# Kernel optimization log

Measured on AMD Instinct MI355X. Metric: run time of the kernel, lower is better.

Reference implementation:

```python
import jax, jax.numpy as jnp
import numpy as np

N_NODES = 50000
N_EDGES = 800000
VOCAB = 4096          # node_emb_size
EMB_DIM = 128         # node_emb_dim
HIDDEN = 128          # hidden_dim -> layer1 out = 2*HIDDEN
N_POS = 1024


def gcn_conv(h, edge_index, W, b, n):
    """PyG GCNConv: lin -> add self loops -> sym-normalized scatter-add -> +bias."""
    h = h @ W                                   # [N, out]
    row, col = edge_index[0], edge_index[1]     # source, target
    loop = jnp.arange(n)
    row = jnp.concatenate([row, loop])
    col = jnp.concatenate([col, loop])
    deg = jax.ops.segment_sum(jnp.ones(row.shape[0], dtype=h.dtype), col, num_segments=n)
    dinv = jnp.where(deg > 0, jax.lax.rsqrt(deg), 0.0)
    norm = dinv[row] * dinv[col]                # [E+N]
    msg = h[row] * norm[:, None]                # gather + scale
    return jax.ops.segment_sum(msg, col, num_segments=n) + b


def setup_inputs() -> dict:
    key = jax.random.key(0)
    ks = jax.random.split(key, 10)
    x = jax.random.randint(ks[0], (N_NODES, 1), 0, VOCAB)
    edge_index = jax.random.randint(ks[1], (2, N_EDGES), 0, N_NODES)
    x_position = jax.random.randint(ks[2], (N_POS,), 0, N_NODES)
    # Embedding init: normal(0, emb_dim^-0.5) per initialize_parameters
    emb = jax.random.normal(ks[3], (VOCAB, EMB_DIM), jnp.float32) * EMB_DIM ** -0.5
    # GCN / linear weights (glorot-ish)
    W1 = jax.random.normal(ks[4], (EMB_DIM, 2 * HIDDEN), jnp.float32) * (EMB_DIM ** -0.5)
    b1 = jnp.zeros((2 * HIDDEN,), jnp.float32)
    W2 = jax.random.normal(ks[5], (2 * HIDDEN, HIDDEN), jnp.float32) * ((2 * HIDDEN) ** -0.5)
    b2 = jnp.zeros((HIDDEN,), jnp.float32)
    Wc = jax.random.normal(ks[6], (HIDDEN, VOCAB), jnp.float32) * (HIDDEN ** -0.5)
    bc = jnp.zeros((VOCAB,), jnp.float32)
    return {"x": x, "edge_index": edge_index, "x_position": x_position,
            "emb": emb, "W1": W1, "b1": b1, "W2": W2, "b2": b2, "Wc": Wc, "bc": bc}


def reference(x, edge_index, x_position, emb, W1, b1, W2, b2, Wc, bc):
    n = x.shape[0]
    h = emb[x[:, 0]]                                   # Embedding + squeeze(1)
    h = jax.nn.relu(gcn_conv(h, edge_index, W1, b1, n))
    z = gcn_conv(h, edge_index, W2, b2, n)             # [N, HIDDEN]
    logits = z @ Wc + bc                               # classifier over all nodes
    # embedding stage: mean of classified rows at x_position, keep dim 0
    return jnp.mean(logits[x_position], axis=0, keepdims=True)  # [1, VOCAB]
```

## Files before the change

### kernel.cpp

```cpp
#include <hip/hip_runtime.h>

constexpr int EMB  = 128;
constexpr int H1D  = 256;
constexpr int H2D  = 128;
constexpr int VOC  = 4096;
constexpr int NSL  = 32;
constexpr int RPB  = 4;

__global__ void kA_init(int* cnt, int* count, unsigned int* flagbits, unsigned int* needw,
                        float* wagg, float* wsum, int* nflag, int* total,
                        const int* __restrict__ xpos,
                        int n, int nwords, int np) {
    int t = threadIdx.x;
    if (blockIdx.x == 0) {
        for (int i = t; i < nwords; i += 256) flagbits[i] = 0u;
        for (int i = t; i < n; i += 256) count[i] = 0;
        __syncthreads();
        for (int i = t; i < np; i += 256) {
            int v = xpos[i];
            atomicAdd(&count[v], 1);
            atomicOr(&flagbits[v >> 5], 1u << (v & 31));
        }
        if (t == 0) { *nflag = 0; *total = 0; }
    } else {
        const int stride = (gridDim.x - 1) * 256;
        const int i0 = (blockIdx.x - 1) * 256 + t;
        for (int i = i0; i < n; i += stride) { cnt[i] = 0; wagg[i] = 0.0f; }
        for (int i = i0; i < nwords; i += stride) needw[i] = 0u;
        for (int i = i0; i < NSL * H1D; i += stride) wsum[i] = 0.0f;
    }
}

constexpr int GEMM_B  = VOC / RPB;
constexpr int HIST_B  = 768;
constexpr int KB_GRID = GEMM_B + HIST_B;
__global__ __launch_bounds__(256) void kB_embW1_hist(
        const float* __restrict__ emb, const float* __restrict__ W1,
        float* __restrict__ embW1,
        const int* __restrict__ row, const int* __restrict__ col,
        const unsigned int* __restrict__ flagbits,
        int* cnt, unsigned int* markw, int ne) {
    int t = threadIdx.x;
    if (blockIdx.x < GEMM_B) {
        __shared__ float er[RPB][EMB];
        int r0 = blockIdx.x * RPB;
        for (int i = t; i < RPB * EMB; i += 256)
            er[i / EMB][i % EMB] = emb[(size_t)r0 * EMB + i];
        __syncthreads();
        float acc[RPB];
#pragma unroll
        for (int rr = 0; rr < RPB; rr++) acc[rr] = 0.0f;
        for (int k = 0; k < EMB; k++) {
            float w = W1[k * H1D + t];
#pragma unroll
            for (int rr = 0; rr < RPB; rr++) acc[rr] += er[rr][k] * w;
        }
#pragma unroll
        for (int rr = 0; rr < RPB; rr++)
            embW1[(size_t)(r0 + rr) * H1D + t] = acc[rr];
    } else {
        const int stride = HIST_B * 256;
        for (int e = (blockIdx.x - GEMM_B) * 256 + t; e < ne; e += stride) {
            int c = col[e];
            atomicAdd(&cnt[c], 1);
            if ((flagbits[c >> 5] >> (c & 31)) & 1u) {
                int r = row[e];
                atomicOr(&markw[r >> 5], 1u << (r & 31));
            }
        }
    }
}

__global__ void k_alloc(unsigned int* needw,
                        const unsigned int* __restrict__ flagbits,
                        const int* __restrict__ cnt, const int* __restrict__ count,
                        const int* __restrict__ x,
                        float* wagg, int* needlist, int* nflag, int* total,
                        int* offs, int* cursor, int2* pk, int n) {
    int v = blockIdx.x * blockDim.x + threadIdx.x;
    int lane = threadIdx.x & 63;
    int cv = 0;
    bool need = false;
    if (v < n) {
        cv = cnt[v];
        float dv = rsqrtf((float)cv + 1.0f);
        int2 p; p.x = x[v]; p.y = __float_as_int(dv);
        pk[v] = p;
        bool mark = (needw[v >> 5] >> (v & 31)) & 1u;
        bool flag = (flagbits[v >> 5] >> (v & 31)) & 1u;
        need = mark || flag;
        if (flag) wagg[v] = (float)count[v] / ((float)cv + 1.0f);
    }
    unsigned long long nm = __ballot(need);
    int wbase = (v & ~63) >> 5;
    if (lane == 0)  needw[wbase]     = (unsigned int)(nm & 0xffffffffu);
    if (lane == 32) needw[wbase + 1] = (unsigned int)(nm >> 32);
    int seg = need ? cv : 0;
    int incl = seg;
#pragma unroll
    for (int d = 1; d < 64; d <<= 1) {
        int t2 = __shfl_up(incl, d);
        if (lane >= d) incl += t2;
    }
    int excl = incl - seg;
    int wave_total = __shfl(incl, 63);
    int rank = __popcll(nm & ((1ull << lane) - 1));
    int wcnt = __popcll(nm);
    int base_id = 0, base_off = 0;
    if (lane == 0) {
        if (wcnt > 0)       base_id  = atomicAdd(nflag, wcnt);
        if (wave_total > 0) base_off = atomicAdd(total, wave_total);
    }
    base_id  = __shfl(base_id, 0);
    base_off = __shfl(base_off, 0);
    if (need) {
        needlist[base_id + rank] = v;
        int o = base_off + excl;
        offs[v] = o;
        cursor[v] = o;
    }
}

__global__ void k_scatter(const int* __restrict__ row, const int* __restrict__ col,
                          const unsigned int* __restrict__ needw,
                          const unsigned int* __restrict__ flagbits,
                          const int* __restrict__ count,
                          const int2* __restrict__ pk,
                          int* cursor, int2* srowp, float* wagg, int ne) {
    int e = blockIdx.x * blockDim.x + threadIdx.x;
    if (e < ne) {
        int c = col[e];
        if ((needw[c >> 5] >> (c & 31)) & 1u) {
            int r = row[e];
            int pos = atomicAdd(&cursor[c], 1);
            int2 pr = pk[r];
            srowp[pos] = pr;
            if ((flagbits[c >> 5] >> (c & 31)) & 1u) {
                float dc = __int_as_float(pk[c].y);
                float dr = __int_as_float(pr.y);
                atomicAdd(&wagg[r], (float)count[c] * dc * dr);
            }
        }
    }
}

__global__ void k_fconv(const int* __restrict__ needlist, const int* __restrict__ nneed_p,
                        const float* __restrict__ wagg, const int* __restrict__ x,
                        const int2* __restrict__ srowp,
                        const int* __restrict__ offs, const int* __restrict__ cnt,
                        const float* __restrict__ embW1, const float* __restrict__ b1,
                        float* __restrict__ wsum) {
    int lane = threadIdx.x & 63;
    int wib  = threadIdx.x >> 6;
    int wid  = blockIdx.x * (blockDim.x >> 6) + wib;
    int nw   = gridDim.x * (blockDim.x >> 6);
    int nn   = *nneed_p;
    const float4* __restrict__ ew = (const float4*)embW1;
    float4 bfrag = ((const float4*)b1)[lane];
    float4 acc2 = {0.0f, 0.0f, 0.0f, 0.0f};

    for (int i = wid; i < nn; i += nw) {
        int v = needlist[i];
        int cv = cnt[v];
        float dv = rsqrtf((float)cv + 1.0f);
        float wa = wagg[v];
        float4 s = ew[(size_t)x[v] * 64 + lane];
        float w0 = dv * dv;
        float4 acc;
        acc.x = bfrag.x + w0 * s.x;
        acc.y = bfrag.y + w0 * s.y;
        acc.z = bfrag.z + w0 * s.z;
        acc.w = bfrag.w + w0 * s.w;
        int start = offs[v], m = cv;
        for (int base = 0; base < m; base += 64) {
            int mm = min(64, m - base);
            int xr = 0; float wr = 0.0f;
            if (lane < mm) {
                int2 pk2 = srowp[start + base + lane];
                xr = pk2.x;
                wr = __int_as_float(pk2.y) * dv;
            }
            int e = 0;
            for (; e + 4 <= mm; e += 4) {
                int i0 = __shfl(xr, e),     i1 = __shfl(xr, e + 1);
                int i2 = __shfl(xr, e + 2), i3 = __shfl(xr, e + 3);
                float q0 = __shfl(wr, e),     q1 = __shfl(wr, e + 1);
                float q2 = __shfl(wr, e + 2), q3 = __shfl(wr, e + 3);
                float4 t0 = ew[(size_t)i0 * 64 + lane];
                float4 t1 = ew[(size_t)i1 * 64 + lane];
                float4 t2 = ew[(size_t)i2 * 64 + lane];
                float4 t3 = ew[(size_t)i3 * 64 + lane];
                acc.x += q0 * t0.x + q1 * t1.x + q2 * t2.x + q3 * t3.x;
                acc.y += q0 * t0.y + q1 * t1.y + q2 * t2.y + q3 * t3.y;
                acc.z += q0 * t0.z + q1 * t1.z + q2 * t2.z + q3 * t3.z;
                acc.w += q0 * t0.w + q1 * t1.w + q2 * t2.w + q3 * t3.w;
            }
            for (; e < mm; e++) {
                int i0 = __shfl(xr, e);
                float q0 = __shfl(wr, e);
                float4 t0 = ew[(size_t)i0 * 64 + lane];
                acc.x += q0 * t0.x;
                acc.y += q0 * t0.y;
                acc.z += q0 * t0.z;
                acc.w += q0 * t0.w;
            }
        }
        acc2.x += wa * fmaxf(acc.x, 0.0f);
        acc2.y += wa * fmaxf(acc.y, 0.0f);
        acc2.z += wa * fmaxf(acc.z, 0.0f);
        acc2.w += wa * fmaxf(acc.w, 0.0f);
    }

    __shared__ float red[4][H1D];
    red[wib][4 * lane + 0] = acc2.x;
    red[wib][4 * lane + 1] = acc2.y;
    red[wib][4 * lane + 2] = acc2.z;
    red[wib][4 * lane + 3] = acc2.w;
    __syncthreads();
    int t = threadIdx.x;
    float ssum = red[0][t] + red[1][t] + red[2][t] + red[3][t];
    atomicAdd(&wsum[(blockIdx.x & (NSL - 1)) * H1D + t], ssum);
}

__global__ void k_zout(const float* __restrict__ wsum, const float* __restrict__ W2,
                       const float* __restrict__ b2, const float* __restrict__ Wc,
                       const float* __restrict__ bc, float* __restrict__ out,
                       float inv_np) {
    __shared__ float ws[H1D];
    __shared__ float z[H2D];
    __shared__ float red[256];
    int t = threadIdx.x;
    float s = 0.0f;
#pragma unroll
    for (int c2 = 0; c2 < NSL; c2++) s += wsum[c2 * H1D + t];
    ws[t] = s;
    __syncthreads();
    if (t < H2D) {
        float acc = 0.0f;
#pragma unroll 8
        for (int k = 0; k < H1D; k++) acc += ws[k] * W2[k * H2D + t];
        z[t] = b2[t] + acc * inv_np;
    }
    __syncthreads();
    int c  = blockIdx.x * 64 + (t & 63);
    int ks = t >> 6;
    float acc = 0.0f;
#pragma unroll 8
    for (int j = ks * 32; j < ks * 32 + 32; j++) acc += z[j] * Wc[(size_t)j * VOC + c];
    red[t] = acc;
    __syncthreads();
    if (t < 64) {
        int cc = blockIdx.x * 64 + t;
        out[cc] = bc[cc] + red[t] + red[t + 64] + red[t + 128] + red[t + 192];
    }
}

extern "C" void kernel_launch(void* const* d_in, const int* in_sizes, int n_in,
                              void* d_out, int out_size, void* d_ws, size_t ws_size,
                              hipStream_t stream) {
    const int n  = in_sizes[0];
    const int ne = in_sizes[1] / 2;
    const int np = in_sizes[2];

    const int*   x    = (const int*)d_in[0];
    const int*   ei   = (const int*)d_in[1];
    const int*   xpos = (const int*)d_in[2];
    const float* emb  = (const float*)d_in[3];
    const float* W1   = (const float*)d_in[4];
    const float* b1   = (const float*)d_in[5];
    const float* W2   = (const float*)d_in[6];
    const float* b2   = (const float*)d_in[7];
    const float* Wc   = (const float*)d_in[8];
    const float* bc   = (const float*)d_in[9];
    float*       out  = (float*)d_out;

    const int* row = ei;
    const int* col = ei + ne;

    char* p = (char*)d_ws;
    auto alloc = [&](size_t bytes) {
        char* r = p;
        p += (bytes + 255) & ~(size_t)255;
        return r;
    };
    const int nb     = (n + 255) / 256;
    const int neb    = (ne + 255) / 256;
    const int nwords = nb * 8;

    int*          cnt      = (int*)alloc((size_t)n * 4);
    int*          offs     = (int*)alloc((size_t)n * 4);
    int*          cursor   = (int*)alloc((size_t)n * 4);
    int*          count    = (int*)alloc((size_t)n * 4);
    int*          needlist = (int*)alloc((size_t)n * 4);
    unsigned int* needw    = (unsigned int*)alloc((size_t)nwords * 4);
    unsigned int* flagbits = (unsigned int*)alloc((size_t)nwords * 4);
    int2*         srowp    = (int2*)alloc((size_t)ne * 8);
    int2*         pk       = (int2*)alloc((size_t)n * 8);
    int*          nflag    = (int*)alloc(256 * 4);
    int*          total    = (int*)alloc(256 * 4);
    float*        wagg     = (float*)alloc((size_t)n * 4);
    float*        embW1    = (float*)alloc((size_t)VOC * H1D * 4);
    float*        wsum     = (float*)alloc((size_t)NSL * H1D * 4);

    kA_init<<<nb, 256, 0, stream>>>(cnt, count, flagbits, needw, wagg, wsum,
                                    nflag, total, xpos, n, nwords, np);
    kB_embW1_hist<<<KB_GRID, 256, 0, stream>>>(emb, W1, embW1, row, col, flagbits,
                                               cnt, needw, ne);
    k_alloc<<<nb, 256, 0, stream>>>(needw, flagbits, cnt, count, x, wagg,
                                    needlist, nflag, total, offs, cursor, pk, n);
    k_scatter<<<neb, 256, 0, stream>>>(row, col, needw, flagbits, count, pk,
                                       cursor, srowp, wagg, ne);
    k_fconv<<<2048, 256, 0, stream>>>(needlist, nflag, wagg, x, srowp, offs, cnt,
                                      embW1, b1, wsum);
    k_zout<<<VOC / 64, 256, 0, stream>>>(wsum, W2, b2, Wc, bc, out, 1.0f / (float)np);
}
```

Before: 183.9 us.

## Replace global atomic degree histogram with range-partitioned LDS histograms

The in-degree histogram is now built with shared-memory counters. Each block owns one of 64 node ranges and one of 4 edge-teams, and writes partial counts to a per-team buffer. k_alloc sums the four partials and writes cnt itself, so zeroing cnt in init is no longer needed. This removes contended global atomics, but every block now rescans its team's quarter of the col array (64 passes over the edges in total), trading atomic traffic for extra reads.

```diff
diff --git a/kernel.cpp b/kernel.cpp
--- a/kernel.cpp
+++ b/kernel.cpp
@@ -7,7 +7,15 @@
 constexpr int NSL  = 32;
 constexpr int RPB  = 4;
 
-__global__ void kA_init(int* cnt, int* count, unsigned int* flagbits, unsigned int* needw,
+constexpr int NRANGE = 64;
+constexpr int RMAX   = 1024;
+constexpr int TEAMS  = 4;
+
+constexpr int GEMM_B  = VOC / RPB;
+constexpr int HIST_B  = NRANGE * TEAMS;
+constexpr int KB_GRID = GEMM_B + HIST_B;
+
+__global__ void kA_init(int* count, unsigned int* flagbits, unsigned int* needw,
                         float* wagg, float* wsum, int* nflag, int* total,
                         const int* __restrict__ xpos,
                         int n, int nwords, int np) {
@@ -25,21 +33,18 @@
     } else {
         const int stride = (gridDim.x - 1) * 256;
         const int i0 = (blockIdx.x - 1) * 256 + t;
-        for (int i = i0; i < n; i += stride) { cnt[i] = 0; wagg[i] = 0.0f; }
+        for (int i = i0; i < n; i += stride) wagg[i] = 0.0f;
         for (int i = i0; i < nwords; i += stride) needw[i] = 0u;
         for (int i = i0; i < NSL * H1D; i += stride) wsum[i] = 0.0f;
     }
 }
 
-constexpr int GEMM_B  = VOC / RPB;
-constexpr int HIST_B  = 768;
-constexpr int KB_GRID = GEMM_B + HIST_B;
 __global__ __launch_bounds__(256) void kB_embW1_hist(
         const float* __restrict__ emb, const float* __restrict__ W1,
         float* __restrict__ embW1,
         const int* __restrict__ row, const int* __restrict__ col,
         const unsigned int* __restrict__ flagbits,
-        int* cnt, unsigned int* markw, int ne) {
+        int* __restrict__ cntp, unsigned int* markw, int ne, int R) {
     int t = threadIdx.x;
     if (blockIdx.x < GEMM_B) {
         __shared__ float er[RPB][EMB];
@@ -59,30 +64,46 @@
         for (int rr = 0; rr < RPB; rr++)
             embW1[(size_t)(r0 + rr) * H1D + t] = acc[rr];
     } else {
-        const int stride = HIST_B * 256;
-        for (int e = (blockIdx.x - GEMM_B) * 256 + t; e < ne; e += stride) {
+        __shared__ int lc[RMAX];
+        int h     = blockIdx.x - GEMM_B;
+        int range = h & (NRANGE - 1);
+        int team  = h / NRANGE;
+        int base  = range * R;
+        for (int i = t; i < R; i += 256) lc[i] = 0;
+        __syncthreads();
+        int q  = (((ne + TEAMS - 1) / TEAMS) + 255) & ~255;
+        int e1 = min(ne, team * q + q);
+        for (int e = team * q + t; e < e1; e += 256) {
             int c = col[e];
-            atomicAdd(&cnt[c], 1);
-            if ((flagbits[c >> 5] >> (c & 31)) & 1u) {
-                int r = row[e];
-                atomicOr(&markw[r >> 5], 1u << (r & 31));
-            }
-        }
+            unsigned int d = (unsigned int)(c - base);
+            if (d < (unsigned int)R) {
+                atomicAdd(&lc[d], 1);
+                if ((flagbits[c >> 5] >> (c & 31)) & 1u) {
+                    int r = row[e];
+                    atomicOr(&markw[r >> 5], 1u << (r & 31));
+                }
+            }
+        }
+        __syncthreads();
+        int s = NRANGE * R;
+        for (int i = t; i < R; i += 256) cntp[team * s + base + i] = lc[i];
     }
 }
 
 __global__ void k_alloc(unsigned int* needw,
                         const unsigned int* __restrict__ flagbits,
-                        const int* __restrict__ cnt, const int* __restrict__ count,
+                        const int* __restrict__ cntp, const int* __restrict__ count,
                         const int* __restrict__ x,
                         float* wagg, int* needlist, int* nflag, int* total,
-                        int* offs, int* cursor, int2* pk, int n) {
+                        int* offs, int* cursor, int2* pk, int* cnt,
+                        int n, int sTeam) {
     int v = blockIdx.x * blockDim.x + threadIdx.x;
     int lane = threadIdx.x & 63;
     int cv = 0;
     bool need = false;
     if (v < n) {
-        cv = cnt[v];
+        cv = cntp[v] + cntp[sTeam + v] + cntp[2 * sTeam + v] + cntp[3 * sTeam + v];
+        cnt[v] = cv;
         float dv = rsqrtf((float)cv + 1.0f);
         int2 p; p.x = x[v]; p.y = __float_as_int(dv);
         pk[v] = p;
@@ -286,6 +307,8 @@
     const int nb     = (n + 255) / 256;
     const int neb    = (ne + 255) / 256;
     const int nwords = nb * 8;
+    const int R      = (n + NRANGE - 1) / NRANGE;
+    const int sTeam  = NRANGE * R;
 
     int*          cnt      = (int*)alloc((size_t)n * 4);
     int*          offs     = (int*)alloc((size_t)n * 4);
@@ -296,18 +319,20 @@
     unsigned int* flagbits = (unsigned int*)alloc((size_t)nwords * 4);
     int2*         srowp    = (int2*)alloc((size_t)ne * 8);
     int2*         pk       = (int2*)alloc((size_t)n * 8);
+    int*          cntp     = (int*)alloc((size_t)TEAMS * sTeam * 4);
     int*          nflag    = (int*)alloc(256 * 4);
     int*          total    = (int*)alloc(256 * 4);
     float*        wagg     = (float*)alloc((size_t)n * 4);
     float*        embW1    = (float*)alloc((size_t)VOC * H1D * 4);
     float*        wsum     = (float*)alloc((size_t)NSL * H1D * 4);
 
-    kA_init<<<nb, 256, 0, stream>>>(cnt, count, flagbits, needw, wagg, wsum,
+    kA_init<<<nb, 256, 0, stream>>>(count, flagbits, needw, wagg, wsum,
                                     nflag, total, xpos, n, nwords, np);
     kB_embW1_hist<<<KB_GRID, 256, 0, stream>>>(emb, W1, embW1, row, col, flagbits,
-                                               cnt, needw, ne);
-    k_alloc<<<nb, 256, 0, stream>>>(needw, flagbits, cnt, count, x, wagg,
-                                    needlist, nflag, total, offs, cursor, pk, n);
+                                               cntp, needw, ne, R);
+    k_alloc<<<nb, 256, 0, stream>>>(needw, flagbits, cntp, count, x, wagg,
+                                    needlist, nflag, total, offs, cursor, pk, cnt,
+                                    n, sTeam);
     k_scatter<<<neb, 256, 0, stream>>>(row, col, needw, flagbits, count, pk,
                                        cursor, srowp, wagg, ne);
     k_fconv<<<2048, 256, 0, stream>>>(needlist, nflag, wagg, x, srowp, offs, cnt,
```

After: 382.8 us. 2.08x slower.
